# Kernel optimization log

Hardware: AMD Instinct MI355X
Metric: run time of the kernel (lower is better)

The kernel has to match this reference:

```python
import jax, jax.numpy as jnp
import numpy as np

E = 23   # unique experts
K = 3    # active experts per token

def setup_inputs() -> dict:
    key = jax.random.key(0)
    ks = jax.random.split(key, 11)
    d, h, B, N = 1024, 768, 16, 196
    s = 0.02  # init scale so sigmoid gate is non-saturated
    return {
        "x":      jax.random.normal(ks[0], (B, N, d), jnp.float32),
        "gate_w": jax.random.normal(ks[1], (d, E), jnp.float32) * s,
        "gate_b": jnp.zeros((E,), jnp.float32),
        "w1":     jax.random.normal(ks[2], (E, d, h), jnp.float32) * s,
        "b1":     jnp.zeros((E, h), jnp.float32),
        "w2":     jax.random.normal(ks[3], (E, h, d), jnp.float32) * s,
        "b2":     jnp.zeros((E, d), jnp.float32),
        "ws1":    jax.random.normal(ks[4], (d, h), jnp.float32) * s,
        "bs1":    jnp.zeros((h,), jnp.float32),
        "ws2":    jax.random.normal(ks[5], (h, d), jnp.float32) * s,
        "bs2":    jnp.zeros((d,), jnp.float32),
    }

def reference(x, gate_w, gate_b, w1, b1, w2, b2, ws1, bs1, ws2, bs2):
    o_shape = x.shape
    xt = x.reshape(-1, o_shape[-1])            # [T, d]
    T = xt.shape[0]

    # gating: sigmoid gate, top-3 (the 'bias' buffer in the source is zeros)
    gw = jax.nn.sigmoid(xt @ gate_w + gate_b)  # [T, E]
    top_vals, top_idx = jax.lax.top_k(gw, K)   # [T, K]
    tw = top_vals / top_vals.sum(-1, keepdims=True)

    # dense combine weights: tw scattered to [T, E] (0 for unselected experts)
    w_dense = jnp.zeros_like(gw).at[jnp.arange(T)[:, None], top_idx].add(tw)

    # expert MLPs (dense-masked equivalent of the grouped dispatch)
    hh = jax.nn.gelu(jnp.einsum('td,edh->teh', xt, w1) + b1, approximate=False)
    eo = jnp.einsum('teh,ehd->ted', hh, w2) + b2          # [T, E, d]

    # shared expert
    shared = jax.nn.gelu(xt @ ws1 + bs1, approximate=False) @ ws2 + bs2

    out = shared + jnp.einsum('ted,te->td', eo, w_dense)  # [T, d]

    # aux load-balancing loss
    gwn = gw / gw.sum(-1, keepdims=True)
    P = gwn.mean(0)                                       # [E]
    counts = jnp.zeros((E,), gw.dtype).at[top_idx.reshape(-1)].add(1.0)
    Fv = E * counts / (K * T)
    aux = (P * Fv).sum()

    return out.reshape(o_shape), aux
```

## Files before the change

### kernel.cpp

```cpp
#include <hip/hip_runtime.h>
#include <hip/hip_bf16.h>

#define T_TOK 3136
#define DDIM  1024
#define HDIM  768
#define NEXP  23
#define TOPK  3
#define MTILE 128
#define NTILE 128
#define KTILE 32
#define LDSB  40
#define MAXTILES 128
#define MAX_SLOTS 16384
#define GATE_BLOCKS 1568
#define NBLK_T 13

typedef __attribute__((ext_vector_type(8))) short  short8;
typedef __attribute__((ext_vector_type(4))) short  short4v;
typedef __attribute__((ext_vector_type(2))) short  short2v;
typedef __attribute__((ext_vector_type(4))) float  floatx4;

__device__ __forceinline__ short f2b(float f) {
    union { float f; unsigned u; } v; v.f = f;
    unsigned r = v.u + 0x7FFFu + ((v.u >> 16) & 1u);
    return (short)(r >> 16);
}
__device__ __forceinline__ float b2f(short s) {
    union { unsigned u; float f; } v; v.u = ((unsigned)(unsigned short)s) << 16; return v.f;
}
__device__ __forceinline__ float gelu_exact(float v) {
    return 0.5f * v * (1.0f + erff(v * 0.70710678118654752f));
}
__device__ __forceinline__ void gld16(const short* g, short* l) {
    __builtin_amdgcn_global_load_lds(
        (const __attribute__((address_space(1))) void*)g,
        (__attribute__((address_space(3))) void*)l, 16, 0, 0);
}

__global__ __launch_bounds__(256) void gwt_kernel(const float* __restrict__ gw, float* __restrict__ gwT) {
    __shared__ float tile[32][33];
    const int kt = blockIdx.x;
    const int tx = threadIdx.x & 31, ty = threadIdx.x >> 5;
    #pragma unroll
    for (int i = 0; i < 4; i++) {
        int k = ty + i * 8;
        tile[k][tx] = (tx < NEXP) ? gw[(size_t)(kt * 32 + k) * NEXP + tx] : 0.f;
    }
    __syncthreads();
    #pragma unroll
    for (int i = 0; i < 4; i++) {
        int e = ty + i * 8;
        if (e < 24) gwT[(size_t)e * DDIM + kt * 32 + tx] = tile[tx][e];
    }
}

__global__ __launch_bounds__(256) void xcvt_kernel(const float* __restrict__ x, short* __restrict__ xb) {
    int i = blockIdx.x * 256 + threadIdx.x;
    float4 v = ((const float4*)x)[i];
    short4v s = { f2b(v.x), f2b(v.y), f2b(v.z), f2b(v.w) };
    ((short4v*)xb)[i] = s;
}

__global__ __launch_bounds__(256) void gate_kernel(
    const float* __restrict__ x, const float* __restrict__ gwT, const float* __restrict__ gb,
    float* __restrict__ gwn, int* __restrict__ top_idx, float* __restrict__ top_w)
{
    const int tid = threadIdx.x;
    const int lane = tid & 63, wave = tid >> 6;
    const int ebase = wave * 6;
    __shared__ float sg[24];

    for (int t = blockIdx.x; t < T_TOK; t += GATE_BLOCKS) {
        const float4* xr4 = (const float4*)(x + (size_t)t * DDIM);
        float4 xv[4];
        #pragma unroll
        for (int j = 0; j < 4; j++) xv[j] = xr4[j * 64 + lane];

        double a0 = 0, a1 = 0, a2 = 0, a3 = 0, a4 = 0, a5 = 0;
        #pragma unroll
        for (int j = 0; j < 4; j++) {
            const float4* gp = (const float4*)gwT + (size_t)ebase * 256 + j * 64 + lane;
            float4 g0 = gp[0 * 256], g1 = gp[1 * 256], g2 = gp[2 * 256];
            float4 g3 = gp[3 * 256], g4 = gp[4 * 256], g5 = gp[5 * 256];
            float4 xj = xv[j];
            a0 += (double)xj.x * g0.x + (double)xj.y * g0.y + (double)xj.z * g0.z + (double)xj.w * g0.w;
            a1 += (double)xj.x * g1.x + (double)xj.y * g1.y + (double)xj.z * g1.z + (double)xj.w * g1.w;
            a2 += (double)xj.x * g2.x + (double)xj.y * g2.y + (double)xj.z * g2.z + (double)xj.w * g2.w;
            a3 += (double)xj.x * g3.x + (double)xj.y * g3.y + (double)xj.z * g3.z + (double)xj.w * g3.w;
            a4 += (double)xj.x * g4.x + (double)xj.y * g4.y + (double)xj.z * g4.z + (double)xj.w * g4.w;
            a5 += (double)xj.x * g5.x + (double)xj.y * g5.y + (double)xj.z * g5.z + (double)xj.w * g5.w;
        }
        #pragma unroll
        for (int off = 32; off > 0; off >>= 1) {
            a0 += __shfl_xor(a0, off);
            a1 += __shfl_xor(a1, off);
            a2 += __shfl_xor(a2, off);
            a3 += __shfl_xor(a3, off);
            a4 += __shfl_xor(a4, off);
            a5 += __shfl_xor(a5, off);
        }

        if (lane == 0) {
            double av[6] = { a0, a1, a2, a3, a4, a5 };
            #pragma unroll
            for (int i = 0; i < 6; i++) {
                int e = ebase + i;
                if (e < NEXP) {
                    float z = (float)av[i] + gb[e];
                    sg[e] = 1.0f / (1.0f + expf(-z));
                }
            }
        }
        __syncthreads();

        if (tid < NEXP) {
            float s = 0.f;
            #pragma unroll
            for (int e = 0; e < NEXP; e++) s += sg[e];
            gwn[(size_t)t * NEXP + tid] = sg[tid] / s;
        }
        if (tid == 0) {
            float v0 = -1.f, v1 = -1.f, v2 = -1.f; int i0 = 0, i1 = 0, i2 = 0;
            for (int e = 0; e < NEXP; e++) {
                float v = sg[e];
                if (v > v0)      { v2 = v1; i2 = i1; v1 = v0; i1 = i0; v0 = v; i0 = e; }
                else if (v > v1) { v2 = v1; i2 = i1; v1 = v; i1 = e; }
                else if (v > v2) { v2 = v; i2 = e; }
            }
            float ts = v0 + v1 + v2;
            top_idx[t * 3 + 0] = i0; top_w[t * 3 + 0] = v0 / ts;
            top_idx[t * 3 + 1] = i1; top_w[t * 3 + 1] = v1 / ts;
            top_idx[t * 3 + 2] = i2; top_w[t * 3 + 2] = v2 / ts;
        }
        __syncthreads();
    }
}

__global__ __launch_bounds__(256) void hist_kernel(
    const int* __restrict__ top_idx, int* __restrict__ block_hist, int* __restrict__ counts)
{
    __shared__ int h[NEXP];
    const int b = blockIdx.x, tid = threadIdx.x;
    if (tid < NEXP) h[tid] = 0;
    __syncthreads();
    int t = b * 256 + tid;
    if (t < T_TOK) {
        atomicAdd(&h[top_idx[t * 3 + 0]], 1);
        atomicAdd(&h[top_idx[t * 3 + 1]], 1);
        atomicAdd(&h[top_idx[t * 3 + 2]], 1);
    }
    __syncthreads();
    if (tid < NEXP) {
        block_hist[b * NEXP + tid] = h[tid];
        atomicAdd(&counts[tid], h[tid]);
    }
}

__global__ __launch_bounds__(256) void offsets_kernel(
    const int* __restrict__ counts, const int* __restrict__ block_hist,
    int* __restrict__ offs, int* __restrict__ ntl, int* __restrict__ block_base,
    int* __restrict__ slot_t, int* __restrict__ tmap_e, int* __restrict__ tmap_b)
{
    __shared__ int soffs[NEXP + 1];
    if (threadIdx.x == 0) {
        int o = 0, ti = 0;
        for (int e = 0; e < NEXP; e++) {
            int nt = (counts[e] + MTILE - 1) / MTILE;
            ntl[e] = nt; offs[e] = o; soffs[e] = o;
            for (int j = 0; j < nt; j++) { tmap_e[ti] = e; tmap_b[ti] = o + j * MTILE; ti++; }
            o += nt * MTILE;
        }
        int nts = (T_TOK + MTILE - 1) / MTILE;
        ntl[NEXP] = nts; offs[NEXP] = o; soffs[NEXP] = o;
        for (int j = 0; j < nts; j++) { tmap_e[ti] = NEXP; tmap_b[ti] = o + j * MTILE; ti++; }
        o += nts * MTILE;
        offs[NEXP + 1] = o;
        ntl[NEXP + 1] = ti;
    }
    __syncthreads();
    if (threadIdx.x < NEXP) {
        int e = threadIdx.x;
        int run = soffs[e];
        for (int b = 0; b < NBLK_T; b++) {
            block_base[b * NEXP + e] = run;
            run += block_hist[b * NEXP + e];
        }
    }
    for (int i = threadIdx.x; i < MAX_SLOTS; i += 256) slot_t[i] = 0;
}

__global__ __launch_bounds__(256) void scatter_kernel(
    const int* __restrict__ top_idx, const int* __restrict__ offs,
    const int* __restrict__ block_base,
    int* __restrict__ slot_t, int* __restrict__ slot_of)
{
    __shared__ int lfill[NEXP];
    const int b = blockIdx.x, tid = threadIdx.x;
    if (tid < NEXP) lfill[tid] = 0;
    __syncthreads();
    int t = b * 256 + tid;
    if (t < T_TOK) {
        #pragma unroll
        for (int k = 0; k < TOPK; k++) {
            int e = top_idx[t * 3 + k];
            int pos = atomicAdd(&lfill[e], 1);
            int s = block_base[b * NEXP + e] + pos;
            slot_t[s] = t;
            slot_of[t * 4 + k] = s;
        }
        int s = offs[NEXP] + t;
        slot_t[s] = t;
        slot_of[t * 4 + 3] = s;
    }
}

__global__ __launch_bounds__(256) void gemm1_kernel(
    const short* __restrict__ xb,
    const float* __restrict__ w1, const float* __restrict__ b1,
    const float* __restrict__ ws1, const float* __restrict__ bs1,
    const int* __restrict__ tmap_e, const int* __restrict__ tmap_b,
    const int* __restrict__ ntl,
    const int* __restrict__ slot_t, short* __restrict__ hh)
{
    if ((int)blockIdx.y >= ntl[NEXP + 1]) return;
    const int e = tmap_e[blockIdx.y];
    const int slot_base = tmap_b[blockIdx.y];
    const int n0 = blockIdx.x * NTILE;
    const float* __restrict__ Wf = (e < NEXP) ? (w1 + (size_t)e * DDIM * HDIM) : ws1;
    const float* __restrict__ Bv = (e < NEXP) ? (b1 + (size_t)e * HDIM) : bs1;

    __shared__ __align__(16) short As[MTILE * KTILE];
    __shared__ __align__(16) short Bs[NTILE * LDSB];
    __shared__ int toks[MTILE];

    const int tid = threadIdx.x;
    for (int i = tid; i < MTILE; i += 256) toks[i] = slot_t[slot_base + i];

    const int lane = tid & 63, wave = tid >> 6;
    const int mbase = (wave & 1) * 64, nbase = (wave >> 1) * 64;
    const int lc = lane & 15, q = lane >> 4;
    const int xq8 = (q ^ ((lc >> 1) & 3)) << 3;

    const int srow = wave * 16 + (lane >> 2);
    const int c8   = (lane & 3) * 8;

    __syncthreads();
    const short* gA0 = xb + (size_t)toks[srow]      * DDIM + c8;
    const short* gA1 = xb + (size_t)toks[64 + srow] * DDIM + c8;
    short* lA0 = As + wave * 512;
    short* lA1 = As + 2048 + wave * 512;

    const int g = wave, cn = lane;
    const float* gW = Wf + (size_t)(8 * g) * HDIM + n0 + 2 * cn;
    const int bws = (g ^ (cn & 3)) << 3;
    short* bw0 = Bs + (2 * cn)     * LDSB + bws;
    short* bw1 = Bs + (2 * cn + 1) * LDSB + bws;

    floatx4 acc[4][4];
    #pragma unroll
    for (int m = 0; m < 4; m++)
        #pragma unroll
        for (int n = 0; n < 4; n++) acc[m][n] = (floatx4)0.f;

    for (int k0 = 0; k0 < DDIM; k0 += KTILE) {
        gld16(gA0 + k0, lA0);
        gld16(gA1 + k0, lA1);
        const float* gp = gW + (size_t)k0 * HDIM;
        float2 f[8];
        #pragma unroll
        for (int j = 0; j < 8; j++) f[j] = *(const float2*)(gp + (size_t)j * HDIM);
        short8 s0, s1;
        #pragma unroll
        for (int j = 0; j < 8; j++) { s0[j] = f2b(f[j].x); s1[j] = f2b(f[j].y); }
        *(short8*)bw0 = s0;
        *(short8*)bw1 = s1;
        __syncthreads();
        short8 af[4], bf[4];
        #pragma unroll
        for (int m = 0; m < 4; m++) af[m] = *(const short8*)&As[(mbase + m * 16 + lc) * KTILE + q * 8];
        #pragma unroll
        for (int n = 0; n < 4; n++) bf[n] = *(const short8*)&Bs[(nbase + n * 16 + lc) * LDSB + xq8];
        #pragma unroll
        for (int m = 0; m < 4; m++)
            #pragma unroll
            for (int n = 0; n < 4; n++)
                acc[m][n] = __builtin_amdgcn_mfma_f32_16x16x32_bf16(af[m], bf[n], acc[m][n], 0, 0, 0);
        __syncthreads();
    }

    #pragma unroll
    for (int n = 0; n < 4; n++) {
        const int col = n0 + nbase + n * 16 + lc;
        const float bb = Bv[col];
        #pragma unroll
        for (int m = 0; m < 4; m++) {
            const int rbase = slot_base + mbase + m * 16 + q * 4;
            #pragma unroll
            for (int r = 0; r < 4; r++) {
                float v = acc[m][n][r] + bb;
                hh[(size_t)(rbase + r) * HDIM + col] = f2b(gelu_exact(v));
            }
        }
    }
}

__global__ __launch_bounds__(256) void gemm2_kernel(
    const short* __restrict__ hh,
    const float* __restrict__ w2, const float* __restrict__ b2,
    const float* __restrict__ ws2, const float* __restrict__ bs2,
    const int* __restrict__ tmap_e, const int* __restrict__ tmap_b,
    const int* __restrict__ ntl,
    short* __restrict__ eo)
{
    if ((int)blockIdx.y >= ntl[NEXP + 1]) return;
    const int e = tmap_e[blockIdx.y];
    const int slot_base = tmap_b[blockIdx.y];
    const int n0 = blockIdx.x * NTILE;
    const float* __restrict__ Wf = (e < NEXP) ? (w2 + (size_t)e * HDIM * DDIM) : ws2;
    const float* __restrict__ Bv = (e < NEXP) ? (b2 + (size_t)e * DDIM) : bs2;

    __shared__ __align__(16) short As[MTILE * KTILE];
    __shared__ __align__(16) short Bs[NTILE * LDSB];

    const int tid = threadIdx.x;
    const int lane = tid & 63, wave = tid >> 6;
    const int mbase = (wave & 1) * 64, nbase = (wave >> 1) * 64;
    const int lc = lane & 15, q = lane >> 4;
    const int xq8 = (q ^ ((lc >> 1) & 3)) << 3;

    const int srow = wave * 16 + (lane >> 2);
    const int c8   = (lane & 3) * 8;

    const short* gA0 = hh + (size_t)(slot_base + srow)      * HDIM + c8;
    const short* gA1 = hh + (size_t)(slot_base + 64 + srow) * HDIM + c8;
    short* lA0 = As + wave * 512;
    short* lA1 = As + 2048 + wave * 512;

    const int g = wave, cn = lane;
    const float* gW = Wf + (size_t)(8 * g) * DDIM + n0 + 2 * cn;
    const int bws = (g ^ (cn & 3)) << 3;
    short* bw0 = Bs + (2 * cn)     * LDSB + bws;
    short* bw1 = Bs + (2 * cn + 1) * LDSB + bws;

    floatx4 acc[4][4];
    #pragma unroll
    for (int m = 0; m < 4; m++)
        #pragma unroll
        for (int n = 0; n < 4; n++) acc[m][n] = (floatx4)0.f;

    for (int k0 = 0; k0 < HDIM; k0 += KTILE) {
        gld16(gA0 + k0, lA0);
        gld16(gA1 + k0, lA1);
        const float* gp = gW + (size_t)k0 * DDIM;
        float2 f[8];
        #pragma unroll
        for (int j = 0; j < 8; j++) f[j] = *(const float2*)(gp + (size_t)j * DDIM);
        short8 s0, s1;
        #pragma unroll
        for (int j = 0; j < 8; j++) { s0[j] = f2b(f[j].x); s1[j] = f2b(f[j].y); }
        *(short8*)bw0 = s0;
        *(short8*)bw1 = s1;
        __syncthreads();
        short8 af[4], bf[4];
        #pragma unroll
        for (int m = 0; m < 4; m++) af[m] = *(const short8*)&As[(mbase + m * 16 + lc) * KTILE + q * 8];
        #pragma unroll
        for (int n = 0; n < 4; n++) bf[n] = *(const short8*)&Bs[(nbase + n * 16 + lc) * LDSB + xq8];
        #pragma unroll
        for (int m = 0; m < 4; m++)
            #pragma unroll
            for (int n = 0; n < 4; n++)
                acc[m][n] = __builtin_amdgcn_mfma_f32_16x16x32_bf16(af[m], bf[n], acc[m][n], 0, 0, 0);
        __syncthreads();
    }

    #pragma unroll
    for (int n = 0; n < 4; n++) {
        const int col = n0 + nbase + n * 16 + lc;
        const float bb = Bv[col];
        #pragma unroll
        for (int m = 0; m < 4; m++) {
            const int rbase = slot_base + mbase + m * 16 + q * 4;
            #pragma unroll
            for (int r = 0; r < 4; r++)
                eo[(size_t)(rbase + r) * DDIM + col] = f2b(acc[m][n][r] + bb);
        }
    }
}

__global__ __launch_bounds__(256) void combine_kernel(
    const short* __restrict__ eo, const float* __restrict__ top_w,
    const int* __restrict__ slot_of, float* __restrict__ out)
{
    const int t = blockIdx.x;
    const int c = threadIdx.x * 4;
    const int s0 = slot_of[t * 4 + 0], s1 = slot_of[t * 4 + 1];
    const int s2 = slot_of[t * 4 + 2], s3 = slot_of[t * 4 + 3];
    const float w0 = top_w[t * 3 + 0], w1 = top_w[t * 3 + 1], w2 = top_w[t * 3 + 2];
    short4v a = *(const short4v*)(eo + (size_t)s0 * DDIM + c);
    short4v b = *(const short4v*)(eo + (size_t)s1 * DDIM + c);
    short4v d = *(const short4v*)(eo + (size_t)s2 * DDIM + c);
    short4v s = *(const short4v*)(eo + (size_t)s3 * DDIM + c);
    float4 o;
    o.x = b2f(s.x) + w0 * b2f(a.x) + w1 * b2f(b.x) + w2 * b2f(d.x);
    o.y = b2f(s.y) + w0 * b2f(a.y) + w1 * b2f(b.y) + w2 * b2f(d.y);
    o.z = b2f(s.z) + w0 * b2f(a.z) + w1 * b2f(b.z) + w2 * b2f(d.z);
    o.w = b2f(s.w) + w0 * b2f(a.w) + w1 * b2f(b.w) + w2 * b2f(d.w);
    *(float4*)(out + (size_t)t * DDIM + c) = o;
}

__global__ __launch_bounds__(256) void preduce_kernel(const float* __restrict__ gwn, float* __restrict__ Pf) {
    __shared__ float sP[NEXP];
    if (threadIdx.x < NEXP) sP[threadIdx.x] = 0.f;
    __syncthreads();
    int t = blockIdx.x * blockDim.x + threadIdx.x;
    if (t < T_TOK) {
        #pragma unroll
        for (int e = 0; e < NEXP; e++) atomicAdd(&sP[e], gwn[(size_t)t * NEXP + e]);
    }
    __syncthreads();
    if (threadIdx.x < NEXP) atomicAdd(&Pf[threadIdx.x], sP[threadIdx.x]);
}

__global__ void aux_kernel(const float* __restrict__ Pf, const int* __restrict__ counts,
                           float* __restrict__ out_aux) {
    if (threadIdx.x == 0 && blockIdx.x == 0) {
        float aux = 0.f;
        for (int e = 0; e < NEXP; e++) {
            float P = Pf[e] / (float)T_TOK;
            float F = (float)NEXP * (float)counts[e] / (float)(TOPK * T_TOK);
            aux += P * F;
        }
        out_aux[0] = aux;
    }
}

extern "C" void kernel_launch(void* const* d_in, const int* in_sizes, int n_in,
                              void* d_out, int out_size, void* d_ws, size_t ws_size,
                              hipStream_t stream)
{
    const float* x   = (const float*)d_in[0];
    const float* gw  = (const float*)d_in[1];
    const float* gb  = (const float*)d_in[2];
    const float* w1  = (const float*)d_in[3];
    const float* b1  = (const float*)d_in[4];
    const float* w2  = (const float*)d_in[5];
    const float* b2  = (const float*)d_in[6];
    const float* ws1 = (const float*)d_in[7];
    const float* bs1 = (const float*)d_in[8];
    const float* ws2 = (const float*)d_in[9];
    const float* bs2 = (const float*)d_in[10];
    float* out = (float*)d_out;

    char* p = (char*)d_ws;
    auto alloc = [&](size_t bytes) -> char* {
        char* r = p; p += (bytes + 255) & ~(size_t)255; return r;
    };
    float* gwn      = (float*)alloc((size_t)T_TOK * NEXP * 4);
    int*   top_idx  = (int*)  alloc((size_t)T_TOK * 3 * 4);
    float* top_w    = (float*)alloc((size_t)T_TOK * 3 * 4);
    int*   meta     = (int*)  alloc(2 * NEXP * 4);
    int*   counts   = meta;
    float* Pf       = (float*)(meta + NEXP);
    int*   offs     = (int*)  alloc((NEXP + 2) * 4);
    int*   ntl      = (int*)  alloc((NEXP + 2) * 4);
    int*   bhist    = (int*)  alloc((size_t)NBLK_T * NEXP * 4);
    int*   bbase    = (int*)  alloc((size_t)NBLK_T * NEXP * 4);
    int*   slot_t   = (int*)  alloc((size_t)MAX_SLOTS * 4);
    int*   slot_of  = (int*)  alloc((size_t)T_TOK * 4 * 4);
    int*   tmap_e   = (int*)  alloc((size_t)MAXTILES * 4);
    int*   tmap_b   = (int*)  alloc((size_t)MAXTILES * 4);
    float* gwT      = (float*)alloc((size_t)24 * DDIM * 4);
    short* xb       = (short*)alloc((size_t)T_TOK * DDIM * 2);
    short* hh       = (short*)alloc((size_t)MAX_SLOTS * HDIM * 2);
    short* eo       = (short*)alloc((size_t)MAX_SLOTS * DDIM * 2);

    hipMemsetAsync(meta, 0, 2 * NEXP * 4, stream);

    gwt_kernel<<<DDIM / 32, 256, 0, stream>>>(gw, gwT);
    xcvt_kernel<<<(T_TOK * DDIM / 4) / 256, 256, 0, stream>>>(x, xb);
    gate_kernel<<<GATE_BLOCKS, 256, 0, stream>>>(x, gwT, gb, gwn, top_idx, top_w);
    hist_kernel<<<NBLK_T, 256, 0, stream>>>(top_idx, bhist, counts);
    offsets_kernel<<<1, 256, 0, stream>>>(counts, bhist, offs, ntl, bbase, slot_t, tmap_e, tmap_b);
    scatter_kernel<<<NBLK_T, 256, 0, stream>>>(top_idx, offs, bbase, slot_t, slot_of);
    gemm1_kernel<<<dim3(HDIM / NTILE, MAXTILES), 256, 0, stream>>>(
        xb, w1, b1, ws1, bs1, tmap_e, tmap_b, ntl, slot_t, hh);
    gemm2_kernel<<<dim3(DDIM / NTILE, MAXTILES), 256, 0, stream>>>(
        hh, w2, b2, ws2, bs2, tmap_e, tmap_b, ntl, eo);
    combine_kernel<<<T_TOK, 256, 0, stream>>>(eo, top_w, slot_of, out);
    preduce_kernel<<<(T_TOK + 255) / 256, 256, 0, stream>>>(gwn, Pf);
    aux_kernel<<<1, 64, 0, stream>>>(Pf, counts, out + (size_t)T_TOK * DDIM);
}
```

Baseline: 424.1 us.

## Double-buffer GEMM tiles and fuse routing, histogram and aux-loss kernels

The expert GEMM kernels now double-buffer their LDS tiles and prefetch weight registers two steps ahead, so global loads overlap the MFMA work with one barrier per k-step. The gate kernel accumulates normalized gate probabilities per block and adds them atomically, which removes the gwn buffer and the preduce pass. Histogram, offsets, scatter and aux-loss computation are merged into a single 1024-thread route kernel, and only the padding slots are zeroed. This cuts launch overhead and memory traffic, but doubles LDS use and serializes routing on one block.

```diff
diff --git a/kernel.cpp b/kernel.cpp
--- a/kernel.cpp
+++ b/kernel.cpp
@@ -13,11 +13,9 @@
 #define MAXTILES 128
 #define MAX_SLOTS 16384
 #define GATE_BLOCKS 1568
-#define NBLK_T 13
 
 typedef __attribute__((ext_vector_type(8))) short  short8;
 typedef __attribute__((ext_vector_type(4))) short  short4v;
-typedef __attribute__((ext_vector_type(2))) short  short2v;
 typedef __attribute__((ext_vector_type(4))) float  floatx4;
 
 __device__ __forceinline__ short f2b(float f) {
@@ -63,12 +61,14 @@
 
 __global__ __launch_bounds__(256) void gate_kernel(
     const float* __restrict__ x, const float* __restrict__ gwT, const float* __restrict__ gb,
-    float* __restrict__ gwn, int* __restrict__ top_idx, float* __restrict__ top_w)
+    float* __restrict__ Pf, int* __restrict__ top_idx, float* __restrict__ top_w)
 {
     const int tid = threadIdx.x;
     const int lane = tid & 63, wave = tid >> 6;
     const int ebase = wave * 6;
     __shared__ float sg[24];
+    __shared__ float accP[NEXP];
+    if (tid < NEXP) accP[tid] = 0.f;
 
     for (int t = blockIdx.x; t < T_TOK; t += GATE_BLOCKS) {
         const float4* xr4 = (const float4*)(x + (size_t)t * DDIM);
@@ -117,7 +117,7 @@
             float s = 0.f;
             #pragma unroll
             for (int e = 0; e < NEXP; e++) s += sg[e];
-            gwn[(size_t)t * NEXP + tid] = sg[tid] / s;
+            accP[tid] += sg[tid] / s;
         }
         if (tid == 0) {
             float v0 = -1.f, v1 = -1.f, v2 = -1.f; int i0 = 0, i1 = 0, i2 = 0;
@@ -134,81 +134,62 @@
         }
         __syncthreads();
     }
-}
-
-__global__ __launch_bounds__(256) void hist_kernel(
-    const int* __restrict__ top_idx, int* __restrict__ block_hist, int* __restrict__ counts)
+    if (tid < NEXP) atomicAdd(&Pf[tid], accP[tid]);
+}
+
+__global__ __launch_bounds__(1024) void route_kernel(
+    const int* __restrict__ top_idx, const float* __restrict__ Pf,
+    int* __restrict__ ntl,
+    int* __restrict__ slot_t, int* __restrict__ slot_of,
+    int* __restrict__ tmap_e, int* __restrict__ tmap_b,
+    float* __restrict__ out_aux)
 {
     __shared__ int h[NEXP];
-    const int b = blockIdx.x, tid = threadIdx.x;
-    if (tid < NEXP) h[tid] = 0;
-    __syncthreads();
-    int t = b * 256 + tid;
-    if (t < T_TOK) {
-        atomicAdd(&h[top_idx[t * 3 + 0]], 1);
-        atomicAdd(&h[top_idx[t * 3 + 1]], 1);
-        atomicAdd(&h[top_idx[t * 3 + 2]], 1);
-    }
-    __syncthreads();
-    if (tid < NEXP) {
-        block_hist[b * NEXP + tid] = h[tid];
-        atomicAdd(&counts[tid], h[tid]);
-    }
-}
-
-__global__ __launch_bounds__(256) void offsets_kernel(
-    const int* __restrict__ counts, const int* __restrict__ block_hist,
-    int* __restrict__ offs, int* __restrict__ ntl, int* __restrict__ block_base,
-    int* __restrict__ slot_t, int* __restrict__ tmap_e, int* __restrict__ tmap_b)
-{
+    __shared__ int lfill[NEXP];
     __shared__ int soffs[NEXP + 1];
-    if (threadIdx.x == 0) {
+    __shared__ int sntl[NEXP + 1];
+    const int tid = threadIdx.x;
+    if (tid < NEXP) { h[tid] = 0; lfill[tid] = 0; }
+    __syncthreads();
+    for (int i = tid; i < T_TOK * 3; i += 1024) atomicAdd(&h[top_idx[i]], 1);
+    __syncthreads();
+    if (tid == 0) {
         int o = 0, ti = 0;
         for (int e = 0; e < NEXP; e++) {
-            int nt = (counts[e] + MTILE - 1) / MTILE;
-            ntl[e] = nt; offs[e] = o; soffs[e] = o;
+            int c = h[e];
+            int nt = (c + MTILE - 1) / MTILE;
+            soffs[e] = o; sntl[e] = nt; ntl[e] = nt;
             for (int j = 0; j < nt; j++) { tmap_e[ti] = e; tmap_b[ti] = o + j * MTILE; ti++; }
             o += nt * MTILE;
         }
         int nts = (T_TOK + MTILE - 1) / MTILE;
-        ntl[NEXP] = nts; offs[NEXP] = o; soffs[NEXP] = o;
+        soffs[NEXP] = o; sntl[NEXP] = nts; ntl[NEXP] = nts;
         for (int j = 0; j < nts; j++) { tmap_e[ti] = NEXP; tmap_b[ti] = o + j * MTILE; ti++; }
-        o += nts * MTILE;
-        offs[NEXP + 1] = o;
         ntl[NEXP + 1] = ti;
-    }
-    __syncthreads();
-    if (threadIdx.x < NEXP) {
-        int e = threadIdx.x;
-        int run = soffs[e];
-        for (int b = 0; b < NBLK_T; b++) {
-            block_base[b * NEXP + e] = run;
-            run += block_hist[b * NEXP + e];
-        }
-    }
-    for (int i = threadIdx.x; i < MAX_SLOTS; i += 256) slot_t[i] = 0;
-}
-
-__global__ __launch_bounds__(256) void scatter_kernel(
-    const int* __restrict__ top_idx, const int* __restrict__ offs,
-    const int* __restrict__ block_base,
-    int* __restrict__ slot_t, int* __restrict__ slot_of)
-{
-    __shared__ int lfill[NEXP];
-    const int b = blockIdx.x, tid = threadIdx.x;
-    if (tid < NEXP) lfill[tid] = 0;
-    __syncthreads();
-    int t = b * 256 + tid;
-    if (t < T_TOK) {
+        float aux = 0.f;
+        for (int e = 0; e < NEXP; e++) {
+            float P = Pf[e] / (float)T_TOK;
+            float F = (float)NEXP * (float)h[e] / (float)(TOPK * T_TOK);
+            aux += P * F;
+        }
+        out_aux[0] = aux;
+    }
+    __syncthreads();
+    for (int e = 0; e <= NEXP; e++) {
+        int cnt = (e < NEXP) ? h[e] : T_TOK;
+        int s0 = soffs[e] + cnt, s1 = soffs[e] + sntl[e] * MTILE;
+        for (int s = s0 + tid; s < s1; s += 1024) slot_t[s] = 0;
+    }
+    for (int t = tid; t < T_TOK; t += 1024) {
         #pragma unroll
         for (int k = 0; k < TOPK; k++) {
             int e = top_idx[t * 3 + k];
             int pos = atomicAdd(&lfill[e], 1);
-            int s = block_base[b * NEXP + e] + pos;
+            int s = soffs[e] + pos;
             slot_t[s] = t;
             slot_of[t * 4 + k] = s;
         }
-        int s = offs[NEXP] + t;
+        int s = soffs[NEXP] + t;
         slot_t[s] = t;
         slot_of[t * 4 + 3] = s;
     }
@@ -229,8 +210,8 @@
     const float* __restrict__ Wf = (e < NEXP) ? (w1 + (size_t)e * DDIM * HDIM) : ws1;
     const float* __restrict__ Bv = (e < NEXP) ? (b1 + (size_t)e * HDIM) : bs1;
 
-    __shared__ __align__(16) short As[MTILE * KTILE];
-    __shared__ __align__(16) short Bs[NTILE * LDSB];
+    __shared__ __align__(16) short As[2][MTILE * KTILE];
+    __shared__ __align__(16) short Bs[2][NTILE * LDSB];
     __shared__ int toks[MTILE];
 
     const int tid = threadIdx.x;
@@ -247,14 +228,12 @@
     __syncthreads();
     const short* gA0 = xb + (size_t)toks[srow]      * DDIM + c8;
     const short* gA1 = xb + (size_t)toks[64 + srow] * DDIM + c8;
-    short* lA0 = As + wave * 512;
-    short* lA1 = As + 2048 + wave * 512;
+    const int lofs0 = wave * 512, lofs1 = 2048 + wave * 512;
 
     const int g = wave, cn = lane;
     const float* gW = Wf + (size_t)(8 * g) * HDIM + n0 + 2 * cn;
     const int bws = (g ^ (cn & 3)) << 3;
-    short* bw0 = Bs + (2 * cn)     * LDSB + bws;
-    short* bw1 = Bs + (2 * cn + 1) * LDSB + bws;
+    const int bofs0 = (2 * cn) * LDSB + bws, bofs1 = (2 * cn + 1) * LDSB + bws;
 
     floatx4 acc[4][4];
     #pragma unroll
@@ -262,24 +241,44 @@
         #pragma unroll
         for (int n = 0; n < 4; n++) acc[m][n] = (floatx4)0.f;
 
-    for (int k0 = 0; k0 < DDIM; k0 += KTILE) {
-        gld16(gA0 + k0, lA0);
-        gld16(gA1 + k0, lA1);
-        const float* gp = gW + (size_t)k0 * HDIM;
-        float2 f[8];
-        #pragma unroll
-        for (int j = 0; j < 8; j++) f[j] = *(const float2*)(gp + (size_t)j * HDIM);
+    const int NT = DDIM / KTILE;
+    float2 f[8];
+    #pragma unroll
+    for (int j = 0; j < 8; j++) f[j] = *(const float2*)(gW + (size_t)j * HDIM);
+    gld16(gA0, &As[0][lofs0]);
+    gld16(gA1, &As[0][lofs1]);
+    {
         short8 s0, s1;
         #pragma unroll
         for (int j = 0; j < 8; j++) { s0[j] = f2b(f[j].x); s1[j] = f2b(f[j].y); }
-        *(short8*)bw0 = s0;
-        *(short8*)bw1 = s1;
-        __syncthreads();
+        *(short8*)&Bs[0][bofs0] = s0;
+        *(short8*)&Bs[0][bofs1] = s1;
+    }
+    #pragma unroll
+    for (int j = 0; j < 8; j++) f[j] = *(const float2*)(gW + (size_t)(KTILE + j) * HDIM);
+    __syncthreads();
+
+    for (int t = 0; t < NT; t++) {
+        const int cur = t & 1;
+        if (t + 1 < NT) {
+            gld16(gA0 + (t + 1) * KTILE, &As[cur ^ 1][lofs0]);
+            gld16(gA1 + (t + 1) * KTILE, &As[cur ^ 1][lofs1]);
+            short8 s0, s1;
+            #pragma unroll
+            for (int j = 0; j < 8; j++) { s0[j] = f2b(f[j].x); s1[j] = f2b(f[j].y); }
+            *(short8*)&Bs[cur ^ 1][bofs0] = s0;
+            *(short8*)&Bs[cur ^ 1][bofs1] = s1;
+        }
+        if (t + 2 < NT) {
+            #pragma unroll
+            for (int j = 0; j < 8; j++)
+                f[j] = *(const float2*)(gW + (size_t)((t + 2) * KTILE + j) * HDIM);
+        }
         short8 af[4], bf[4];
         #pragma unroll
-        for (int m = 0; m < 4; m++) af[m] = *(const short8*)&As[(mbase + m * 16 + lc) * KTILE + q * 8];
-        #pragma unroll
-        for (int n = 0; n < 4; n++) bf[n] = *(const short8*)&Bs[(nbase + n * 16 + lc) * LDSB + xq8];
+        for (int m = 0; m < 4; m++) af[m] = *(const short8*)&As[cur][(mbase + m * 16 + lc) * KTILE + q * 8];
+        #pragma unroll
+        for (int n = 0; n < 4; n++) bf[n] = *(const short8*)&Bs[cur][(nbase + n * 16 + lc) * LDSB + xq8];
         #pragma unroll
         for (int m = 0; m < 4; m++)
             #pragma unroll
@@ -319,8 +318,8 @@
     const float* __restrict__ Wf = (e < NEXP) ? (w2 + (size_t)e * HDIM * DDIM) : ws2;
     const float* __restrict__ Bv = (e < NEXP) ? (b2 + (size_t)e * DDIM) : bs2;
 
-    __shared__ __align__(16) short As[MTILE * KTILE];
-    __shared__ __align__(16) short Bs[NTILE * LDSB];
+    __shared__ __align__(16) short As[2][MTILE * KTILE];
+    __shared__ __align__(16) short Bs[2][NTILE * LDSB];
 
     const int tid = threadIdx.x;
     const int lane = tid & 63, wave = tid >> 6;
@@ -333,14 +332,12 @@
 
     const short* gA0 = hh + (size_t)(slot_base + srow)      * HDIM + c8;
     const short* gA1 = hh + (size_t)(slot_base + 64 + srow) * HDIM + c8;
-    short* lA0 = As + wave * 512;
-    short* lA1 = As + 2048 + wave * 512;
+    const int lofs0 = wave * 512, lofs1 = 2048 + wave * 512;
 
     const int g = wave, cn = lane;
     const float* gW = Wf + (size_t)(8 * g) * DDIM + n0 + 2 * cn;
     const int bws = (g ^ (cn & 3)) << 3;
-    short* bw0 = Bs + (2 * cn)     * LDSB + bws;
-    short* bw1 = Bs + (2 * cn + 1) * LDSB + bws;
+    const int bofs0 = (2 * cn) * LDSB + bws, bofs1 = (2 * cn + 1) * LDSB + bws;
 
     floatx4 acc[4][4];
     #pragma unroll
@@ -348,24 +345,44 @@
         #pragma unroll
         for (int n = 0; n < 4; n++) acc[m][n] = (floatx4)0.f;
 
-    for (int k0 = 0; k0 < HDIM; k0 += KTILE) {
-        gld16(gA0 + k0, lA0);
-        gld16(gA1 + k0, lA1);
-        const float* gp = gW + (size_t)k0 * DDIM;
-        float2 f[8];
-        #pragma unroll
-        for (int j = 0; j < 8; j++) f[j] = *(const float2*)(gp + (size_t)j * DDIM);
+    const int NT = HDIM / KTILE;
+    float2 f[8];
+    #pragma unroll
+    for (int j = 0; j < 8; j++) f[j] = *(const float2*)(gW + (size_t)j * DDIM);
+    gld16(gA0, &As[0][lofs0]);
+    gld16(gA1, &As[0][lofs1]);
+    {
         short8 s0, s1;
         #pragma unroll
         for (int j = 0; j < 8; j++) { s0[j] = f2b(f[j].x); s1[j] = f2b(f[j].y); }
-        *(short8*)bw0 = s0;
-        *(short8*)bw1 = s1;
-        __syncthreads();
+        *(short8*)&Bs[0][bofs0] = s0;
+        *(short8*)&Bs[0][bofs1] = s1;
+    }
+    #pragma unroll
+    for (int j = 0; j < 8; j++) f[j] = *(const float2*)(gW + (size_t)(KTILE + j) * DDIM);
+    __syncthreads();
+
+    for (int t = 0; t < NT; t++) {
+        const int cur = t & 1;
+        if (t + 1 < NT) {
+            gld16(gA0 + (t + 1) * KTILE, &As[cur ^ 1][lofs0]);
+            gld16(gA1 + (t + 1) * KTILE, &As[cur ^ 1][lofs1]);
+            short8 s0, s1;
+            #pragma unroll
+            for (int j = 0; j < 8; j++) { s0[j] = f2b(f[j].x); s1[j] = f2b(f[j].y); }
+            *(short8*)&Bs[cur ^ 1][bofs0] = s0;
+            *(short8*)&Bs[cur ^ 1][bofs1] = s1;
+        }
+        if (t + 2 < NT) {
+            #pragma unroll
+            for (int j = 0; j < 8; j++)
+                f[j] = *(const float2*)(gW + (size_t)((t + 2) * KTILE + j) * DDIM);
+        }
         short8 af[4], bf[4];
         #pragma unroll
-        for (int m = 0; m < 4; m++) af[m] = *(const short8*)&As[(mbase + m * 16 + lc) * KTILE + q * 8];
-        #pragma unroll
-        for (int n = 0; n < 4; n++) bf[n] = *(const short8*)&Bs[(nbase + n * 16 + lc) * LDSB + xq8];
+        for (int m = 0; m < 4; m++) af[m] = *(const short8*)&As[cur][(mbase + m * 16 + lc) * KTILE + q * 8];
+        #pragma unroll
+        for (int n = 0; n < 4; n++) bf[n] = *(const short8*)&Bs[cur][(nbase + n * 16 + lc) * LDSB + xq8];
         #pragma unroll
         for (int m = 0; m < 4; m++)
             #pragma unroll
@@ -409,32 +426,6 @@
     *(float4*)(out + (size_t)t * DDIM + c) = o;
 }
 
-__global__ __launch_bounds__(256) void preduce_kernel(const float* __restrict__ gwn, float* __restrict__ Pf) {
-    __shared__ float sP[NEXP];
-    if (threadIdx.x < NEXP) sP[threadIdx.x] = 0.f;
-    __syncthreads();
-    int t = blockIdx.x * blockDim.x + threadIdx.x;
-    if (t < T_TOK) {
-        #pragma unroll
-        for (int e = 0; e < NEXP; e++) atomicAdd(&sP[e], gwn[(size_t)t * NEXP + e]);
-    }
-    __syncthreads();
-    if (threadIdx.x < NEXP) atomicAdd(&Pf[threadIdx.x], sP[threadIdx.x]);
-}
-
-__global__ void aux_kernel(const float* __restrict__ Pf, const int* __restrict__ counts,
-                           float* __restrict__ out_aux) {
-    if (threadIdx.x == 0 && blockIdx.x == 0) {
-        float aux = 0.f;
-        for (int e = 0; e < NEXP; e++) {
-            float P = Pf[e] / (float)T_TOK;
-            float F = (float)NEXP * (float)counts[e] / (float)(TOPK * T_TOK);
-            aux += P * F;
-        }
-        out_aux[0] = aux;
-    }
-}
-
 extern "C" void kernel_launch(void* const* d_in, const int* in_sizes, int n_in,
                               void* d_out, int out_size, void* d_ws, size_t ws_size,
                               hipStream_t stream)
@@ -456,16 +447,10 @@
     auto alloc = [&](size_t bytes) -> char* {
         char* r = p; p += (bytes + 255) & ~(size_t)255; return r;
     };
-    float* gwn      = (float*)alloc((size_t)T_TOK * NEXP * 4);
     int*   top_idx  = (int*)  alloc((size_t)T_TOK * 3 * 4);
     float* top_w    = (float*)alloc((size_t)T_TOK * 3 * 4);
-    int*   meta     = (int*)  alloc(2 * NEXP * 4);
-    int*   counts   = meta;
-    float* Pf       = (float*)(meta + NEXP);
-    int*   offs     = (int*)  alloc((NEXP + 2) * 4);
+    float* Pf       = (float*)alloc(NEXP * 4);
     int*   ntl      = (int*)  alloc((NEXP + 2) * 4);
-    int*   bhist    = (int*)  alloc((size_t)NBLK_T * NEXP * 4);
-    int*   bbase    = (int*)  alloc((size_t)NBLK_T * NEXP * 4);
     int*   slot_t   = (int*)  alloc((size_t)MAX_SLOTS * 4);
     int*   slot_of  = (int*)  alloc((size_t)T_TOK * 4 * 4);
     int*   tmap_e   = (int*)  alloc((size_t)MAXTILES * 4);
@@ -475,19 +460,16 @@
     short* hh       = (short*)alloc((size_t)MAX_SLOTS * HDIM * 2);
     short* eo       = (short*)alloc((size_t)MAX_SLOTS * DDIM * 2);
 
-    hipMemsetAsync(meta, 0, 2 * NEXP * 4, stream);
+    hipMemsetAsync(Pf, 0, NEXP * 4, stream);
 
     gwt_kernel<<<DDIM / 32, 256, 0, stream>>>(gw, gwT);
     xcvt_kernel<<<(T_TOK * DDIM / 4) / 256, 256, 0, stream>>>(x, xb);
-    gate_kernel<<<GATE_BLOCKS, 256, 0, stream>>>(x, gwT, gb, gwn, top_idx, top_w);
-    hist_kernel<<<NBLK_T, 256, 0, stream>>>(top_idx, bhist, counts);
-    offsets_kernel<<<1, 256, 0, stream>>>(counts, bhist, offs, ntl, bbase, slot_t, tmap_e, tmap_b);
-    scatter_kernel<<<NBLK_T, 256, 0, stream>>>(top_idx, offs, bbase, slot_t, slot_of);
+    gate_kernel<<<GATE_BLOCKS, 256, 0, stream>>>(x, gwT, gb, Pf, top_idx, top_w);
+    route_kernel<<<1, 1024, 0, stream>>>(top_idx, Pf, ntl, slot_t, slot_of,
+                                         tmap_e, tmap_b, out + (size_t)T_TOK * DDIM);
     gemm1_kernel<<<dim3(HDIM / NTILE, MAXTILES), 256, 0, stream>>>(
         xb, w1, b1, ws1, bs1, tmap_e, tmap_b, ntl, slot_t, hh);
     gemm2_kernel<<<dim3(DDIM / NTILE, MAXTILES), 256, 0, stream>>>(
         hh, w2, b2, ws2, bs2, tmap_e, tmap_b, ntl, eo);
     combine_kernel<<<T_TOK, 256, 0, stream>>>(eo, top_w, slot_of, out);
-    preduce_kernel<<<(T_TOK + 255) / 256, 256, 0, stream>>>(gwn, Pf);
-    aux_kernel<<<1, 64, 0, stream>>>(Pf, counts, out + (size_t)T_TOK * DDIM);
-}
+}
```

Result: faster. 383.3 us (-9.6%).
